# Optimization experiments

Hardware: AMD Instinct MI355X
Metric: run time of the kernel (lower is better)

## Reference

```python
import jax, jax.numpy as jnp
import numpy as np
from jax import lax

VOCAB, EMB, HID, TAGS = 50000, 300, 512, 50
T, B = 256, 64
H = HID // 2  # per-direction LSTM hidden


def _lstm(xs, W_ih, W_hh, b_ih, b_hh):
    # xs: [T, B, E]; PyTorch gate order i, f, g, o
    xp = jnp.einsum('tbe,ge->tbg', xs, W_ih) + b_ih  # precompute input projection

    def step(carry, x_t):
        h, c = carry
        gates = x_t + h @ W_hh.T + b_hh
        i, f, g, o = jnp.split(gates, 4, axis=-1)
        c = jax.nn.sigmoid(f) * c + jax.nn.sigmoid(i) * jnp.tanh(g)
        h = jax.nn.sigmoid(o) * jnp.tanh(c)
        return (h, c), h

    h0 = jnp.zeros((xs.shape[1], H), xs.dtype)
    _, hs = lax.scan(step, (h0, h0), xp)
    return hs  # [T, B, H]


def setup_inputs() -> dict:
    key = jax.random.key(0)
    ks = jax.random.split(key, 16)
    s_emb = 1.0
    s_lstm = 1.0 / np.sqrt(H)
    inp = {
        'x': jax.random.randint(ks[0], (T, B), 0, VOCAB),
        'y': jax.random.randint(ks[1], (T, B), 0, TAGS),
        'mask': jnp.ones((T, B), dtype=bool),
        'emb': jax.random.normal(ks[2], (VOCAB, EMB), jnp.float32) * s_emb,
        'W_ih_f': jax.random.uniform(ks[3], (4 * H, EMB), jnp.float32, -s_lstm, s_lstm),
        'W_hh_f': jax.random.uniform(ks[4], (4 * H, H), jnp.float32, -s_lstm, s_lstm),
        'b_ih_f': jax.random.uniform(ks[5], (4 * H,), jnp.float32, -s_lstm, s_lstm),
        'b_hh_f': jax.random.uniform(ks[6], (4 * H,), jnp.float32, -s_lstm, s_lstm),
        'W_ih_b': jax.random.uniform(ks[7], (4 * H, EMB), jnp.float32, -s_lstm, s_lstm),
        'W_hh_b': jax.random.uniform(ks[8], (4 * H, H), jnp.float32, -s_lstm, s_lstm),
        'b_ih_b': jax.random.uniform(ks[9], (4 * H,), jnp.float32, -s_lstm, s_lstm),
        'b_hh_b': jax.random.uniform(ks[10], (4 * H,), jnp.float32, -s_lstm, s_lstm),
        'W_out': jax.random.normal(ks[11], (TAGS, HID), jnp.float32) * 0.02,
        'b_out': jnp.zeros((TAGS,), jnp.float32),
        'start_trans': jax.random.uniform(ks[12], (TAGS,), jnp.float32, -0.1, 0.1),
        'end_trans': jax.random.uniform(ks[13], (TAGS,), jnp.float32, -0.1, 0.1),
        'trans': jax.random.uniform(ks[14], (TAGS, TAGS), jnp.float32, -0.1, 0.1),
    }
    return inp


def _emissions(x, emb, W_ih_f, W_hh_f, b_ih_f, b_hh_f, W_ih_b, W_hh_b, b_ih_b, b_hh_b, W_out, b_out):
    e = emb[x]                                   # [T, B, EMB]
    h_f = _lstm(e, W_ih_f, W_hh_f, b_ih_f, b_hh_f)
    h_b = _lstm(e[::-1], W_ih_b, W_hh_b, b_ih_b, b_hh_b)[::-1]
    h = jnp.concatenate([h_f, h_b], axis=-1)    # [T, B, HID]; dropout in eval mode = identity
    return jnp.einsum('tbh,kh->tbk', h, W_out) + b_out  # [T, B, TAGS]


def _crf_loss(em, y, mask, start_trans, end_trans, trans):
    maskf = mask.astype(em.dtype)
    tt = jnp.arange(1, T)
    bb = jnp.arange(B)
    # numerator: score of the gold path (torchcrf _compute_score)
    num = start_trans[y[0]] + em[0, bb, y[0]]
    num = num + (trans[y[:-1], y[1:]] * maskf[1:]).sum(0)
    num = num + (em[tt[:, None], bb[None, :], y[1:]] * maskf[1:]).sum(0)
    last_idx = mask.astype(jnp.int32).sum(0) - 1
    num = num + end_trans[y[last_idx, bb]]
    # denominator: forward algorithm (log-sum-exp DP)
    def fstep(score, inp):
        em_t, m_t = inp
        nxt = jax.nn.logsumexp(score[:, :, None] + trans[None] + em_t[:, None, :], axis=1)
        return jnp.where(m_t[:, None], nxt, score), None
    score0 = start_trans[None] + em[0]          # [B, TAGS]
    score, _ = lax.scan(fstep, score0, (em[1:], mask[1:]))
    denom = jax.nn.logsumexp(score + end_trans[None], axis=-1)
    return -(num - denom).sum()                 # loss = -llh (sum reduction)


def _crf_decode(em, mask, start_trans, end_trans, trans):
    def vstep(score, inp):
        em_t, m_t = inp
        combo = score[:, :, None] + trans[None]  # [B, prev, cur]
        idx = combo.argmax(1)
        nxt = combo.max(1) + em_t
        return jnp.where(m_t[:, None], nxt, score), idx
    score0 = start_trans[None] + em[0]
    score, history = lax.scan(vstep, score0, (em[1:], mask[1:]))  # history: [T-1, B, TAGS]
    last = jnp.argmax(score + end_trans[None], axis=-1)           # [B]
    def bstep(cur, inp):
        hist_t, m_t = inp
        prev = jnp.take_along_axis(hist_t, cur[:, None], axis=1)[:, 0]
        return jnp.where(m_t, prev, cur), cur
    tag0, rest = lax.scan(bstep, last, (history, mask[1:]), reverse=True)
    return jnp.concatenate([tag0[None], rest], axis=0)            # [T, B] int


def reference(x, y, mask, emb, W_ih_f, W_hh_f, b_ih_f, b_hh_f, W_ih_b, W_hh_b, b_ih_b, b_hh_b, W_out, b_out, start_trans, end_trans, trans):
    em = _emissions(x, emb, W_ih_f, W_hh_f, b_ih_f, b_hh_f, W_ih_b, W_hh_b, b_ih_b, b_hh_b, W_out, b_out)
    loss = _crf_loss(em, y, mask, start_trans, end_trans, trans)
    pred = _crf_decode(em, mask, start_trans, end_trans, trans)
    return (loss, pred)
```

## Files before the change

### kernel.cpp

```cpp
#include <hip/hip_runtime.h>
#include <math.h>

#define T_LEN 256
#define BATCH 64
#define NEMB  300
#define NHID  256
#define NG4   1024
#define NTAGS 50

static constexpr size_t XP_OFF  = 0;
static constexpr size_t XP_SZ   = (size_t)2 * T_LEN * BATCH * NG4;
static constexpr size_t HC_OFF  = XP_OFF + XP_SZ;
static constexpr size_t HC_SZ   = (size_t)T_LEN * BATCH * 512;
static constexpr size_t C_OFF   = HC_OFF + HC_SZ;
static constexpr size_t C_SZ    = (size_t)2 * BATCH * NHID;
static constexpr size_t EM_OFF  = C_OFF + C_SZ;
static constexpr size_t EM_SZ   = (size_t)T_LEN * BATCH * NTAGS;
static constexpr size_t LLH_OFF = EM_OFF + EM_SZ;

__global__ __launch_bounds__(256)
void k_xp(const int* __restrict__ x, const float* __restrict__ emb,
          const float* __restrict__ Wf, const float* __restrict__ Wb,
          const float* __restrict__ bihf, const float* __restrict__ bhhf,
          const float* __restrict__ bihb, const float* __restrict__ bhhb,
          float* __restrict__ xp) {
    __shared__ float As[8 * 136];
    __shared__ float Ws[8 * 136];
    __shared__ int   xrow[128];

    const int tid  = threadIdx.x;
    const int row0 = blockIdx.x * 128;
    const int col0 = blockIdx.y * 128;
    const int dir  = col0 >> 10;
    const int g0   = col0 & 1023;
    const float* __restrict__ W   = dir ? Wb   : Wf;
    const float* __restrict__ bih = dir ? bihb : bihf;
    const float* __restrict__ bhh = dir ? bhhb : bhhf;

    if (tid < 128) xrow[tid] = x[row0 + tid];
    __syncthreads();

    float acc[8][8];
#pragma unroll
    for (int i = 0; i < 8; i++)
#pragma unroll
        for (int j = 0; j < 8; j++) acc[i][j] = 0.f;

    const int ty = tid >> 4;
    const int tx = tid & 15;

    for (int kc = 0; kc < NEMB; kc += 8) {
#pragma unroll
        for (int q = 0; q < 4; q++) {
            int idx = tid + 256 * q;
            int r   = idx >> 3;
            int kk  = idx & 7;
            int k   = kc + kk;
            float av = 0.f, wv = 0.f;
            if (k < NEMB) {
                av = emb[(size_t)xrow[r] * NEMB + k];
                wv = W[(size_t)(g0 + r) * NEMB + k];
            }
            As[kk * 136 + r] = av;
            Ws[kk * 136 + r] = wv;
        }
        __syncthreads();
#pragma unroll
        for (int kk = 0; kk < 8; kk++) {
            float4 a0 = *(const float4*)&As[kk * 136 + 8 * ty];
            float4 a1 = *(const float4*)&As[kk * 136 + 8 * ty + 4];
            float4 b0 = *(const float4*)&Ws[kk * 136 + 8 * tx];
            float4 b1 = *(const float4*)&Ws[kk * 136 + 8 * tx + 4];
            float a[8] = {a0.x,a0.y,a0.z,a0.w,a1.x,a1.y,a1.z,a1.w};
            float w[8] = {b0.x,b0.y,b0.z,b0.w,b1.x,b1.y,b1.z,b1.w};
#pragma unroll
            for (int i = 0; i < 8; i++)
#pragma unroll
                for (int j = 0; j < 8; j++) acc[i][j] += a[i] * w[j];
        }
        __syncthreads();
    }

#pragma unroll
    for (int i = 0; i < 8; i++) {
        size_t row = (size_t)(row0 + 8 * ty + i);
        size_t base = ((size_t)dir * (T_LEN * BATCH) + row) * NG4 + g0 + 8 * tx;
#pragma unroll
        for (int j = 0; j < 8; j++) {
            int g = g0 + 8 * tx + j;
            xp[base + j] = acc[i][j] + bih[g] + bhh[g];
        }
    }
}

__global__ __launch_bounds__(256)
void k_step(const float* __restrict__ xp, const float* __restrict__ Whf,
            const float* __restrict__ Whb, float* __restrict__ hcat,
            float* __restrict__ c, int s) {
    const int blk  = blockIdx.x;
    const int dir  = blk >> 7;
    const int part = blk & 127;
    const int j0   = part * 2;
    const int tid  = threadIdx.x;
    const int b    = tid >> 2;
    const int l    = tid & 3;
    const int t    = dir ? (T_LEN - 1 - s) : s;
    const float* __restrict__ Wh = dir ? Whb : Whf;

    float acc[2][4];
#pragma unroll
    for (int jj = 0; jj < 2; jj++)
#pragma unroll
        for (int g = 0; g < 4; g++) acc[jj][g] = 0.f;

    if (s > 0) {
        const int tprev = dir ? t + 1 : t - 1;
        const float4* __restrict__ hrow =
            (const float4*)(hcat + ((size_t)tprev * BATCH + b) * 512 + dir * NHID);
#pragma unroll
        for (int i = 0; i < 16; i++) {
            const int m = l + 4 * i;
            float4 h4 = hrow[m];
#pragma unroll
            for (int jj = 0; jj < 2; jj++) {
#pragma unroll
                for (int g = 0; g < 4; g++) {
                    const float4* w4 = (const float4*)(Wh + (size_t)(g * NHID + j0 + jj) * NHID);
                    float4 w = w4[m];
                    acc[jj][g] += h4.x * w.x + h4.y * w.y + h4.z * w.z + h4.w * w.w;
                }
            }
        }
    }
#pragma unroll
    for (int jj = 0; jj < 2; jj++)
#pragma unroll
        for (int g = 0; g < 4; g++) {
            float v = acc[jj][g];
            v += __shfl_xor(v, 1);
            v += __shfl_xor(v, 2);
            acc[jj][g] = v;
        }

    if (l == 0) {
        const size_t xpo = ((size_t)dir * (T_LEN * BATCH) + (size_t)t * BATCH + b) * NG4;
#pragma unroll
        for (int jj = 0; jj < 2; jj++) {
            const int j = j0 + jj;
            float gi = xp[xpo + 0 * NHID + j] + acc[jj][0];
            float gf = xp[xpo + 1 * NHID + j] + acc[jj][1];
            float gg = xp[xpo + 2 * NHID + j] + acc[jj][2];
            float go = xp[xpo + 3 * NHID + j] + acc[jj][3];
            float ii = 1.f / (1.f + expf(-gi));
            float ff = 1.f / (1.f + expf(-gf));
            float tg = tanhf(gg);
            float oo = 1.f / (1.f + expf(-go));
            const size_t co = ((size_t)dir * BATCH + b) * NHID + j;
            float cold = (s > 0) ? c[co] : 0.f;
            float cn = ff * cold + ii * tg;
            c[co] = cn;
            hcat[((size_t)t * BATCH + b) * 512 + dir * NHID + j] = oo * tanhf(cn);
        }
    }
}

__global__ __launch_bounds__(256)
void k_em(const float* __restrict__ hcat, const float* __restrict__ Wout,
          const float* __restrict__ bout, float* __restrict__ em) {
    __shared__ float Ws[52 * 128];
    __shared__ float ht[64 * 129];
    const int t   = blockIdx.x;
    const int tid = threadIdx.x;
    const int b   = tid & 63;
    const int tg  = tid >> 6;
    const int tagbase = tg * 13;

    float acc[13];
#pragma unroll
    for (int i = 0; i < 13; i++) acc[i] = 0.f;

    for (int k0 = 0; k0 < 512; k0 += 128) {
        __syncthreads();
#pragma unroll
        for (int q = 0; q < 25; q++) {
            int idx = tid + 256 * q;
            if (idx < 6400) {
                int tag = idx >> 7, kk = idx & 127;
                Ws[tag * 128 + kk] = Wout[(size_t)tag * 512 + k0 + kk];
            }
        }
#pragma unroll
        for (int q = 0; q < 32; q++) {
            int idx = tid + 256 * q;
            int bb = idx >> 7, kk = idx & 127;
            ht[bb * 129 + kk] = hcat[((size_t)t * BATCH + bb) * 512 + k0 + kk];
        }
        __syncthreads();
        for (int kk = 0; kk < 128; kk++) {
            float hv = ht[b * 129 + kk];
#pragma unroll
            for (int i = 0; i < 13; i++)
                acc[i] += hv * Ws[(tagbase + i) * 128 + kk];
        }
    }
#pragma unroll
    for (int i = 0; i < 13; i++) {
        int tag = tagbase + i;
        if (tag < NTAGS)
            em[((size_t)t * BATCH + b) * NTAGS + tag] = acc[i] + bout[tag];
    }
}

__global__ __launch_bounds__(64)
void k_crf_loss(const float* __restrict__ em, const int* __restrict__ y,
                const float* __restrict__ st, const float* __restrict__ et,
                const float* __restrict__ tr, float* __restrict__ llh) {
    __shared__ float trs[2500];
    __shared__ float score[NTAGS];
    __shared__ float red[64];
    const int b   = blockIdx.x;
    const int tid = threadIdx.x;

#pragma unroll
    for (int q = 0; q < 40; q++) {
        int idx = tid + 64 * q;
        if (idx < 2500) trs[idx] = tr[idx];
    }
    __syncthreads();

    float part = 0.f;
    for (int t = tid; t < T_LEN; t += 64) {
        int yt = y[t * BATCH + b];
        if (t == 0) {
            part += st[yt] + em[(size_t)b * NTAGS + yt];
        } else {
            int yp = y[(t - 1) * BATCH + b];
            part += trs[yp * NTAGS + yt] + em[((size_t)t * BATCH + b) * NTAGS + yt];
        }
    }
    red[tid] = part;
    __syncthreads();
    for (int off = 32; off > 0; off >>= 1) {
        if (tid < off) red[tid] += red[tid + off];
        __syncthreads();
    }

    if (tid < NTAGS) score[tid] = st[tid] + em[(size_t)b * NTAGS + tid];
    __syncthreads();

    for (int t = 1; t < T_LEN; t++) {
        float ns = 0.f;
        if (tid < NTAGS) {
            float m = -1e30f;
            for (int p = 0; p < NTAGS; p++) {
                float v = score[p] + trs[p * NTAGS + tid];
                m = fmaxf(m, v);
            }
            float ssum = 0.f;
            for (int p = 0; p < NTAGS; p++) {
                float v = score[p] + trs[p * NTAGS + tid];
                ssum += expf(v - m);
            }
            ns = m + logf(ssum) + em[((size_t)t * BATCH + b) * NTAGS + tid];
        }
        __syncthreads();
        if (tid < NTAGS) score[tid] = ns;
        __syncthreads();
    }

    if (tid == 0) {
        float m = -1e30f;
        for (int cc = 0; cc < NTAGS; cc++) m = fmaxf(m, score[cc] + et[cc]);
        float ssum = 0.f;
        for (int cc = 0; cc < NTAGS; cc++) ssum += expf(score[cc] + et[cc] - m);
        float denom = m + logf(ssum);
        float num = red[0] + et[y[(T_LEN - 1) * BATCH + b]];
        llh[b] = num - denom;
    }
}

__global__ __launch_bounds__(64)
void k_viterbi(const float* __restrict__ em, const float* __restrict__ st,
               const float* __restrict__ et, const float* __restrict__ tr,
               float* __restrict__ out) {
    __shared__ float trs[2500];
    __shared__ float score[NTAGS];
    __shared__ unsigned char hist[(T_LEN - 1) * NTAGS];
    const int b   = blockIdx.x;
    const int tid = threadIdx.x;

#pragma unroll
    for (int q = 0; q < 40; q++) {
        int idx = tid + 64 * q;
        if (idx < 2500) trs[idx] = tr[idx];
    }
    if (tid < NTAGS) score[tid] = st[tid] + em[(size_t)b * NTAGS + tid];
    __syncthreads();

    for (int t = 1; t < T_LEN; t++) {
        float ns = 0.f;
        int am = 0;
        if (tid < NTAGS) {
            float m = -1e30f;
            for (int p = 0; p < NTAGS; p++) {
                float v = score[p] + trs[p * NTAGS + tid];
                if (v > m) { m = v; am = p; }
            }
            ns = m + em[((size_t)t * BATCH + b) * NTAGS + tid];
        }
        __syncthreads();
        if (tid < NTAGS) {
            score[tid] = ns;
            hist[(t - 1) * NTAGS + tid] = (unsigned char)am;
        }
        __syncthreads();
    }

    if (tid == 0) {
        float m = -1e30f;
        int cur = 0;
        for (int cc = 0; cc < NTAGS; cc++) {
            float v = score[cc] + et[cc];
            if (v > m) { m = v; cur = cc; }
        }
        out[1 + (T_LEN - 1) * BATCH + b] = (float)cur;
        for (int t = T_LEN - 2; t >= 0; t--) {
            cur = hist[t * NTAGS + cur];
            out[1 + t * BATCH + b] = (float)cur;
        }
    }
}

__global__ __launch_bounds__(64)
void k_loss_final(const float* __restrict__ llh, float* __restrict__ out) {
    __shared__ float red[64];
    const int tid = threadIdx.x;
    red[tid] = llh[tid];
    __syncthreads();
    for (int off = 32; off > 0; off >>= 1) {
        if (tid < off) red[tid] += red[tid + off];
        __syncthreads();
    }
    if (tid == 0) out[0] = -red[0];
}

extern "C" void kernel_launch(void* const* d_in, const int* in_sizes, int n_in,
                              void* d_out, int out_size, void* d_ws, size_t ws_size,
                              hipStream_t stream) {
    const int*   x    = (const int*)d_in[0];
    const int*   y    = (const int*)d_in[1];
    const float* emb  = (const float*)d_in[3];
    const float* Wihf = (const float*)d_in[4];
    const float* Whhf = (const float*)d_in[5];
    const float* bihf = (const float*)d_in[6];
    const float* bhhf = (const float*)d_in[7];
    const float* Wihb = (const float*)d_in[8];
    const float* Whhb = (const float*)d_in[9];
    const float* bihb = (const float*)d_in[10];
    const float* bhhb = (const float*)d_in[11];
    const float* Wout = (const float*)d_in[12];
    const float* bout = (const float*)d_in[13];
    const float* st   = (const float*)d_in[14];
    const float* et   = (const float*)d_in[15];
    const float* tr   = (const float*)d_in[16];

    float* out  = (float*)d_out;
    float* ws   = (float*)d_ws;
    float* xp   = ws + XP_OFF;
    float* hcat = ws + HC_OFF;
    float* c    = ws + C_OFF;
    float* em   = ws + EM_OFF;
    float* llh  = ws + LLH_OFF;

    dim3 g1(128, 16);
    hipLaunchKernelGGL(k_xp, g1, dim3(256), 0, stream,
                       x, emb, Wihf, Wihb, bihf, bhhf, bihb, bhhb, xp);

    for (int s = 0; s < T_LEN; s++)
        hipLaunchKernelGGL(k_step, dim3(256), dim3(256), 0, stream,
                           xp, Whhf, Whhb, hcat, c, s);

    hipLaunchKernelGGL(k_em, dim3(T_LEN), dim3(256), 0, stream, hcat, Wout, bout, em);

    hipLaunchKernelGGL(k_crf_loss, dim3(BATCH), dim3(64), 0, stream, em, y, st, et, tr, llh);

    hipLaunchKernelGGL(k_viterbi, dim3(BATCH), dim3(64), 0, stream, em, st, et, tr, out);

    hipLaunchKernelGGL(k_loss_final, dim3(1), dim3(64), 0, stream, llh, out);
}
```

Baseline: 3.457 ms.

## Replace per-step LSTM launches with persistent kernel using flag-based inter-block sync

The 256 per-timestep kernel launches are replaced by one persistent kernel of 256 workgroups that loops over time. Blocks exchange hidden state through a double-buffered global array and per-block progress flags polled with atomics. W_hh rows stay resident in registers and the cell state in registers, while h is staged in rotated shared memory to avoid bank conflicts. This removes launch overhead and repeated weight reloads, but relies on all 256 blocks being co-resident and adds spin-wait synchronization cost each step.

After: 13.23 ms. 283% more time.

```diff
diff --git a/kernel.cpp b/kernel.cpp
--- a/kernel.cpp
+++ b/kernel.cpp
@@ -12,11 +12,19 @@
 static constexpr size_t XP_SZ   = (size_t)2 * T_LEN * BATCH * NG4;
 static constexpr size_t HC_OFF  = XP_OFF + XP_SZ;
 static constexpr size_t HC_SZ   = (size_t)T_LEN * BATCH * 512;
-static constexpr size_t C_OFF   = HC_OFF + HC_SZ;
-static constexpr size_t C_SZ    = (size_t)2 * BATCH * NHID;
-static constexpr size_t EM_OFF  = C_OFF + C_SZ;
+static constexpr size_t HX_OFF  = HC_OFF + HC_SZ;
+static constexpr size_t HX_SZ   = (size_t)2 * 2 * BATCH * NHID;
+static constexpr size_t EM_OFF  = HX_OFF + HX_SZ;
 static constexpr size_t EM_SZ   = (size_t)T_LEN * BATCH * NTAGS;
 static constexpr size_t LLH_OFF = EM_OFF + EM_SZ;
+static constexpr size_t FLG_OFF = LLH_OFF + 64;
+
+__global__ __launch_bounds__(256)
+void k_init(float* __restrict__ ws) {
+    unsigned int* f = (unsigned int*)(ws + FLG_OFF);
+    int i = blockIdx.x * 256 + threadIdx.x;
+    if (i < 4096) f[i] = 0u;
+}
 
 __global__ __launch_bounds__(256)
 void k_xp(const int* __restrict__ x, const float* __restrict__ emb,
@@ -93,73 +101,139 @@
     }
 }
 
-__global__ __launch_bounds__(256)
-void k_step(const float* __restrict__ xp, const float* __restrict__ Whf,
+__global__ __launch_bounds__(256, 2)
+void k_lstm(const float* __restrict__ xp, const float* __restrict__ Whf,
             const float* __restrict__ Whb, float* __restrict__ hcat,
-            float* __restrict__ c, int s) {
-    const int blk  = blockIdx.x;
-    const int dir  = blk >> 7;
-    const int part = blk & 127;
-    const int j0   = part * 2;
-    const int tid  = threadIdx.x;
-    const int b    = tid >> 2;
-    const int l    = tid & 3;
-    const int t    = dir ? (T_LEN - 1 - s) : s;
-    const float* __restrict__ Wh = dir ? Whb : Whf;
-
-    float acc[2][4];
-#pragma unroll
-    for (int jj = 0; jj < 2; jj++)
-#pragma unroll
-        for (int g = 0; g < 4; g++) acc[jj][g] = 0.f;
-
-    if (s > 0) {
-        const int tprev = dir ? t + 1 : t - 1;
-        const float4* __restrict__ hrow =
-            (const float4*)(hcat + ((size_t)tprev * BATCH + b) * 512 + dir * NHID);
-#pragma unroll
-        for (int i = 0; i < 16; i++) {
-            const int m = l + 4 * i;
-            float4 h4 = hrow[m];
-#pragma unroll
-            for (int jj = 0; jj < 2; jj++) {
-#pragma unroll
-                for (int g = 0; g < 4; g++) {
-                    const float4* w4 = (const float4*)(Wh + (size_t)(g * NHID + j0 + jj) * NHID);
-                    float4 w = w4[m];
-                    acc[jj][g] += h4.x * w.x + h4.y * w.y + h4.z * w.z + h4.w * w.w;
+            float* __restrict__ hx, unsigned int* __restrict__ flg) {
+    __shared__ float hs[BATCH * NHID];
+
+    const int wg    = blockIdx.x;
+    const int dir   = wg >> 7;
+    const int wslot = wg & 127;
+    const int j0    = wslot * 2;
+    const int tid   = threadIdx.x;
+    const int w     = tid >> 6;
+    const int lane  = tid & 63;
+    const int rg    = w & 1;
+    const int bhalf = w >> 1;
+    const int kthr  = lane >> 3;
+    const int bthr  = lane & 7;
+    const int j     = j0 + rg;
+
+    const float* __restrict__ Wh  = dir ? Whb : Whf;
+    const float* __restrict__ xpd = xp + (size_t)dir * (T_LEN * BATCH) * NG4;
+    float* __restrict__ hxd = hx + (size_t)dir * (2 * BATCH * NHID);
+    unsigned int* __restrict__ flgd = flg + (size_t)dir * 128 * 16;
+
+    float wreg[4][32];
+#pragma unroll
+    for (int g = 0; g < 4; ++g) {
+        const float4* src = (const float4*)(Wh + ((size_t)(g * 256 + j)) * 256 + kthr * 32);
+#pragma unroll
+        for (int q = 0; q < 8; ++q) {
+            float4 v = src[q];
+            wreg[g][q * 4 + 0] = v.x;
+            wreg[g][q * 4 + 1] = v.y;
+            wreg[g][q * 4 + 2] = v.z;
+            wreg[g][q * 4 + 3] = v.w;
+        }
+    }
+    float creg[4] = {0.f, 0.f, 0.f, 0.f};
+
+    for (int s = 0; s < T_LEN; ++s) {
+        const int t = dir ? (T_LEN - 1 - s) : s;
+
+        float xpv[4][4];
+        if (kthr == 0) {
+#pragma unroll
+            for (int bi = 0; bi < 4; ++bi) {
+                const int b = bhalf * 32 + bthr * 4 + bi;
+                const float* xr = xpd + ((size_t)t * BATCH + b) * NG4 + j;
+#pragma unroll
+                for (int g = 0; g < 4; ++g) xpv[g][bi] = xr[g * 256];
+            }
+        }
+
+        float acc[4][4];
+#pragma unroll
+        for (int g = 0; g < 4; ++g)
+#pragma unroll
+            for (int bi = 0; bi < 4; ++bi) acc[g][bi] = 0.f;
+
+        if (s > 0) {
+            if (tid < 128) {
+                while (__hip_atomic_load(&flgd[tid * 16], __ATOMIC_RELAXED,
+                                         __HIP_MEMORY_SCOPE_AGENT) < (unsigned)s) {
+                    __builtin_amdgcn_s_sleep(2);
                 }
             }
-        }
-    }
-#pragma unroll
-    for (int jj = 0; jj < 2; jj++)
-#pragma unroll
-        for (int g = 0; g < 4; g++) {
-            float v = acc[jj][g];
-            v += __shfl_xor(v, 1);
-            v += __shfl_xor(v, 2);
-            acc[jj][g] = v;
-        }
-
-    if (l == 0) {
-        const size_t xpo = ((size_t)dir * (T_LEN * BATCH) + (size_t)t * BATCH + b) * NG4;
-#pragma unroll
-        for (int jj = 0; jj < 2; jj++) {
-            const int j = j0 + jj;
-            float gi = xp[xpo + 0 * NHID + j] + acc[jj][0];
-            float gf = xp[xpo + 1 * NHID + j] + acc[jj][1];
-            float gg = xp[xpo + 2 * NHID + j] + acc[jj][2];
-            float go = xp[xpo + 3 * NHID + j] + acc[jj][3];
-            float ii = 1.f / (1.f + expf(-gi));
-            float ff = 1.f / (1.f + expf(-gf));
-            float tg = tanhf(gg);
-            float oo = 1.f / (1.f + expf(-go));
-            const size_t co = ((size_t)dir * BATCH + b) * NHID + j;
-            float cold = (s > 0) ? c[co] : 0.f;
-            float cn = ff * cold + ii * tg;
-            c[co] = cn;
-            hcat[((size_t)t * BATCH + b) * 512 + dir * NHID + j] = oo * tanhf(cn);
+            __syncthreads();
+
+            const float* hsrc = hxd + (size_t)((s - 1) & 1) * (BATCH * NHID);
+#pragma unroll 4
+            for (int r = 0; r < 64; ++r) {
+                float v = __hip_atomic_load(&hsrc[r * 256 + tid], __ATOMIC_RELAXED,
+                                            __HIP_MEMORY_SCOPE_AGENT);
+                const int phys = r * 256 + (tid & ~31) + (((tid & 31) + 4 * ((r >> 2) & 7)) & 31);
+                hs[phys] = v;
+            }
+            __syncthreads();
+
+#pragma unroll
+            for (int bi = 0; bi < 4; ++bi) {
+                const int b = bhalf * 32 + bthr * 4 + bi;
+                const float* hb = &hs[b * 256 + kthr * 32];
+                const int rot = (b >> 2) & 7;
+#pragma unroll
+                for (int c8 = 0; c8 < 8; ++c8) {
+                    const float4 h4 = *(const float4*)&hb[4 * ((c8 + rot) & 7)];
+#pragma unroll
+                    for (int g = 0; g < 4; ++g) {
+                        acc[g][bi] += h4.x * wreg[g][4 * c8 + 0]
+                                    + h4.y * wreg[g][4 * c8 + 1]
+                                    + h4.z * wreg[g][4 * c8 + 2]
+                                    + h4.w * wreg[g][4 * c8 + 3];
+                    }
+                }
+            }
+#pragma unroll
+            for (int g = 0; g < 4; ++g)
+#pragma unroll
+                for (int bi = 0; bi < 4; ++bi) {
+                    float v = acc[g][bi];
+                    v += __shfl_xor(v, 8);
+                    v += __shfl_xor(v, 16);
+                    v += __shfl_xor(v, 32);
+                    acc[g][bi] = v;
+                }
+        }
+
+        if (kthr == 0) {
+#pragma unroll
+            for (int bi = 0; bi < 4; ++bi) {
+                const int b = bhalf * 32 + bthr * 4 + bi;
+                float gi = acc[0][bi] + xpv[0][bi];
+                float gf = acc[1][bi] + xpv[1][bi];
+                float gg = acc[2][bi] + xpv[2][bi];
+                float go = acc[3][bi] + xpv[3][bi];
+                float ig = 1.f / (1.f + expf(-gi));
+                float fg = 1.f / (1.f + expf(-gf));
+                float tg = tanhf(gg);
+                float og = 1.f / (1.f + expf(-go));
+                float cn = fg * creg[bi] + ig * tg;
+                creg[bi] = cn;
+                float hv = og * tanhf(cn);
+                hcat[((size_t)t * BATCH + b) * 512 + dir * NHID + j] = hv;
+                __hip_atomic_store(&hxd[(size_t)(s & 1) * (BATCH * NHID) + b * NHID + j],
+                                   hv, __ATOMIC_RELAXED, __HIP_MEMORY_SCOPE_AGENT);
+            }
+        }
+
+        if (s < T_LEN - 1) {
+            __syncthreads();
+            if (tid == 0)
+                __hip_atomic_store(&flgd[wslot * 16], (unsigned)(s + 1),
+                                   __ATOMIC_RELEASE, __HIP_MEMORY_SCOPE_AGENT);
         }
     }
 }
@@ -368,17 +442,19 @@
     float* ws   = (float*)d_ws;
     float* xp   = ws + XP_OFF;
     float* hcat = ws + HC_OFF;
-    float* c    = ws + C_OFF;
+    float* hx   = ws + HX_OFF;
     float* em   = ws + EM_OFF;
     float* llh  = ws + LLH_OFF;
+    unsigned int* flg = (unsigned int*)(ws + FLG_OFF);
+
+    hipLaunchKernelGGL(k_init, dim3(16), dim3(256), 0, stream, ws);
 
     dim3 g1(128, 16);
     hipLaunchKernelGGL(k_xp, g1, dim3(256), 0, stream,
                        x, emb, Wihf, Wihb, bihf, bhhf, bihb, bhhb, xp);
 
-    for (int s = 0; s < T_LEN; s++)
-        hipLaunchKernelGGL(k_step, dim3(256), dim3(256), 0, stream,
-                           xp, Whhf, Whhb, hcat, c, s);
+    hipLaunchKernelGGL(k_lstm, dim3(256), dim3(256), 0, stream,
+                       xp, Whhf, Whhb, hcat, hx, flg);
 
     hipLaunchKernelGGL(k_em, dim3(T_LEN), dim3(256), 0, stream, hcat, Wout, bout, em);
 
```
